# Optimization experiments

Measured on AMD Instinct MI355X. Metric: run time of the kernel, lower is better.

Reference implementation:

```python
import jax, jax.numpy as jnp
import numpy as np

IN_F, HID, N_CLS = 128, 256, 2
N_NODES, N_EDGES = 50000, 800000


def setup_inputs() -> dict:
    key = jax.random.key(0)
    ks = jax.random.split(key, 8)
    x = jax.random.normal(ks[0], (N_NODES, IN_F), dtype=jnp.float32)
    edge_index = jax.random.randint(ks[1], (2, N_EDGES), 0, N_NODES, dtype=jnp.int64)
    # Linear params (torch nn.Linear: y = x @ W.T + b), uniform(-1/sqrt(fan_in), ..)
    def lin(k, out_f, in_f):
        k1, k2 = jax.random.split(k)
        bound = 1.0 / np.sqrt(in_f)
        W = jax.random.uniform(k1, (out_f, in_f), minval=-bound, maxval=bound, dtype=jnp.float32)
        b = jax.random.uniform(k2, (out_f,), minval=-bound, maxval=bound, dtype=jnp.float32)
        return W, b
    W1, b1 = lin(ks[2], HID, IN_F)
    W2, b2 = lin(ks[3], HID // 2, HID)
    W3, b3 = lin(ks[4], N_CLS, HID // 2)
    return {"x": x, "edge_index": edge_index, "n_nodes": N_NODES,
            "W1": W1, "b1": b1, "W2": W2, "b2": b2, "W3": W3, "b3": b3}


def _gcn_layer(x, row, col, deg_inv, n_nodes, W, b):
    # gather neighbor features, scatter-add into destinations, degree-normalize
    agg = jax.ops.segment_sum(x[row], col, num_segments=n_nodes)  # [N, F]
    agg = agg * deg_inv[:, None]
    return agg @ W.T + b


def reference(x, edge_index, n_nodes, W1, b1, W2, b2, W3, b3):
    row, col = edge_index[0], edge_index[1]
    deg = jax.ops.segment_sum(jnp.ones_like(col, dtype=x.dtype), col, num_segments=n_nodes)
    deg_inv = 1.0 / jnp.maximum(deg, 1.0)  # bincount().clamp(min=1)
    h = jax.nn.relu(_gcn_layer(x, row, col, deg_inv, n_nodes, W1, b1))
    # dropout is identity in eval mode
    h = jax.nn.relu(_gcn_layer(h, row, col, deg_inv, n_nodes, W2, b2))
    return h @ W3.T + b3  # [N, num_classes]
```

## Files before the change

### kernel.cpp

```cpp
#include <hip/hip_runtime.h>
#include <hip/hip_fp16.h>

#define IN_F 128
#define HID 256
#define HID2 128
#define MAXDEG 64
#define NPART 8

typedef __attribute__((ext_vector_type(8))) _Float16 f16x8;
typedef __attribute__((ext_vector_type(4))) float f32x4;

__global__ __launch_bounds__(256) void prep(
        const float* __restrict__ x,
        const float* __restrict__ W1, const float* __restrict__ W2,
        ushort* __restrict__ xh, ushort* __restrict__ w1h, ushort* __restrict__ w1l,
        ushort* __restrict__ w2h, ushort* __restrict__ w2l,
        int* __restrict__ fill, int N) {
    int gid = blockIdx.x * 256 + threadIdx.x, gsz = gridDim.x * 256;
    for (int i = gid; i < N; i += gsz) fill[i] = 0;
    int t8 = N * IN_F / 8;
    for (int i = gid; i < t8; i += gsz) {
        const float4* s4 = (const float4*)x + (size_t)i * 2;
        float4 f0 = s4[0], f1 = s4[1];
        uint4 o;
        o.x = __half_as_ushort(__float2half(f0.x)) | ((unsigned)__half_as_ushort(__float2half(f0.y)) << 16);
        o.y = __half_as_ushort(__float2half(f0.z)) | ((unsigned)__half_as_ushort(__float2half(f0.w)) << 16);
        o.z = __half_as_ushort(__float2half(f1.x)) | ((unsigned)__half_as_ushort(__float2half(f1.y)) << 16);
        o.w = __half_as_ushort(__float2half(f1.z)) | ((unsigned)__half_as_ushort(__float2half(f1.w)) << 16);
        ((uint4*)xh)[i] = o;
    }
    int nw = HID * IN_F + HID2 * HID;
    for (int i = gid; i < nw; i += gsz) {
        bool first = i < HID * IN_F;
        int j = first ? i : i - HID * IN_F;
        float f = first ? W1[j] : W2[j];
        __half h = __float2half(f);
        __half lo = __float2half(f - __half2float(h));
        if (first) { w1h[j] = __half_as_ushort(h); w1l[j] = __half_as_ushort(lo); }
        else       { w2h[j] = __half_as_ushort(h); w2l[j] = __half_as_ushort(lo); }
    }
}

__global__ __launch_bounds__(256) void fill_csr(const int* __restrict__ row,
                                                const int* __restrict__ col,
                                                int* __restrict__ fill,
                                                ushort* __restrict__ csr,
                                                int E, int npp) {
    int part = blockIdx.x & (NPART - 1);
    int bi   = blockIdx.x >> 3;
    int bpp  = gridDim.x >> 3;
    int lo = part * npp, hi = lo + npp;
    for (int e = bi * 256 + threadIdx.x; e < E; e += bpp * 256) {
        int c = col[e];
        if (c >= lo && c < hi) {
            int p = atomicAdd(&fill[c], 1);
            if (p < MAXDEG) csr[(size_t)c * MAXDEG + p] = (ushort)row[e];
        }
    }
}

__device__ __forceinline__ void add4h(float4& a, uint2 v) {
    float2 f0 = __half22float2(*(const __half2*)&v.x);
    float2 f1 = __half22float2(*(const __half2*)&v.y);
    a.x += f0.x; a.y += f0.y; a.z += f1.x; a.w += f1.y;
}

__global__ __launch_bounds__(256) void agg_gather(const ushort* __restrict__ xh,
                                                  const int* __restrict__ deg,
                                                  const ushort* __restrict__ csr,
                                                  ushort* __restrict__ outh, int N) {
    int w = threadIdx.x >> 6, lane = threadIdx.x & 63;
    int n = blockIdx.x * 4 + w;
    if (n >= N) return;
    int d = deg[n]; if (d > MAXDEG) d = MAXDEG;
    int s = n * MAXDEG, e = s + d;
    int half = lane >> 5, l = lane & 31;
    const uint2* xv = (const uint2*)xh;
    float4 a0 = {0,0,0,0}, a1 = {0,0,0,0}, a2 = {0,0,0,0}, a3 = {0,0,0,0};
    int i = s;
    for (; i + 7 < e; i += 8) {
        int s0 = csr[i + half], s1 = csr[i + 2 + half];
        int s2 = csr[i + 4 + half], s3 = csr[i + 6 + half];
        uint2 v0 = xv[(size_t)s0 * 32 + l];
        uint2 v1 = xv[(size_t)s1 * 32 + l];
        uint2 v2 = xv[(size_t)s2 * 32 + l];
        uint2 v3 = xv[(size_t)s3 * 32 + l];
        add4h(a0, v0); add4h(a1, v1); add4h(a2, v2); add4h(a3, v3);
    }
    for (; i + 1 < e; i += 2) {
        add4h(a0, xv[(size_t)csr[i + half] * 32 + l]);
    }
    if (i < e && half == 0) {
        add4h(a0, xv[(size_t)csr[i] * 32 + l]);
    }
    a0.x += a1.x + a2.x + a3.x; a0.y += a1.y + a2.y + a3.y;
    a0.z += a1.z + a2.z + a3.z; a0.w += a1.w + a2.w + a3.w;
    a0.x += __shfl_xor(a0.x, 32, 64);
    a0.y += __shfl_xor(a0.y, 32, 64);
    a0.z += __shfl_xor(a0.z, 32, 64);
    a0.w += __shfl_xor(a0.w, 32, 64);
    if (half == 0) {
        float dinv = 1.f / fmaxf((float)d, 1.f);
        uint2 o;
        o.x = __half_as_ushort(__float2half(a0.x * dinv)) |
              ((unsigned)__half_as_ushort(__float2half(a0.y * dinv)) << 16);
        o.y = __half_as_ushort(__float2half(a0.z * dinv)) |
              ((unsigned)__half_as_ushort(__float2half(a0.w * dinv)) << 16);
        ((uint2*)outh)[(size_t)n * 32 + l] = o;
    }
}

__global__ __launch_bounds__(256, 2) void gemm_fused(const ushort* __restrict__ A,
                                                  const ushort* __restrict__ W1h,
                                                  const ushort* __restrict__ W1l,
                                                  const ushort* __restrict__ W2h,
                                                  const ushort* __restrict__ W2l,
                                                  const float* __restrict__ b1,
                                                  ushort* __restrict__ Z,
                                                  int M) {
    __shared__ _Float16 hs[64][HID + 8];
    int t = threadIdx.x;
    int wv = t >> 6, l = t & 63;
    int r = l & 15, q = l >> 4;
    int m0 = blockIdx.x * 64;
    const _Float16* Af = (const _Float16*)A;

    {
        int n0 = wv * 64;
        f16x8 WAh[4][4], WAl[4][4];
#pragma unroll
        for (int k4 = 0; k4 < 4; k4++) {
            int kf = k4 * 32 + q * 8;
#pragma unroll
            for (int j = 0; j < 4; j++) {
                size_t wo = (size_t)(n0 + 16 * j + r) * IN_F + kf;
                WAh[k4][j] = *(const f16x8*)((const _Float16*)W1h + wo);
                WAl[k4][j] = *(const f16x8*)((const _Float16*)W1l + wo);
            }
        }
        asm volatile("" ::: "memory");
        f32x4 acc[4][4];
#pragma unroll
        for (int i = 0; i < 4; i++)
#pragma unroll
            for (int j = 0; j < 4; j++) acc[i][j] = (f32x4){0.f, 0.f, 0.f, 0.f};
#pragma unroll
        for (int k4 = 0; k4 < 4; k4++) {
            int kf = k4 * 32 + q * 8;
            f16x8 a[4];
#pragma unroll
            for (int i = 0; i < 4; i++) {
                int m = m0 + 16 * i + r;
                if (m > M - 1) m = M - 1;
                a[i] = *(const f16x8*)(Af + (size_t)m * IN_F + kf);
            }
#pragma unroll
            for (int i = 0; i < 4; i++)
#pragma unroll
                for (int j = 0; j < 4; j++) {
                    acc[i][j] = __builtin_amdgcn_mfma_f32_16x16x32_f16(a[i], WAh[k4][j], acc[i][j], 0, 0, 0);
                    acc[i][j] = __builtin_amdgcn_mfma_f32_16x16x32_f16(a[i], WAl[k4][j], acc[i][j], 0, 0, 0);
                }
        }
#pragma unroll
        for (int j = 0; j < 4; j++) {
            int n = n0 + 16 * j + r;
            float bo = b1[n];
#pragma unroll
            for (int i = 0; i < 4; i++)
#pragma unroll
                for (int reg = 0; reg < 4; reg++) {
                    int mr = 16 * i + q * 4 + reg;
                    hs[mr][n] = (_Float16)fmaxf(acc[i][j][reg] + bo, 0.f);
                }
        }
    }
    __syncthreads();

    {
        int mb = (wv >> 1) * 32, n0 = (wv & 1) * 64;
        f32x4 acc[2][4];
#pragma unroll
        for (int i = 0; i < 2; i++)
#pragma unroll
            for (int j = 0; j < 4; j++) acc[i][j] = (f32x4){0.f, 0.f, 0.f, 0.f};
#pragma unroll
        for (int khalf = 0; khalf < 2; khalf++) {
            f16x8 WBh[4][4], WBl[4][4];
#pragma unroll
            for (int k4 = 0; k4 < 4; k4++) {
                int kf = khalf * 128 + k4 * 32 + q * 8;
#pragma unroll
                for (int j = 0; j < 4; j++) {
                    size_t wo = (size_t)(n0 + 16 * j + r) * HID + kf;
                    WBh[k4][j] = *(const f16x8*)((const _Float16*)W2h + wo);
                    WBl[k4][j] = *(const f16x8*)((const _Float16*)W2l + wo);
                }
            }
            asm volatile("" ::: "memory");
#pragma unroll
            for (int k4 = 0; k4 < 4; k4++) {
                int kf = khalf * 128 + k4 * 32 + q * 8;
                f16x8 a[2];
#pragma unroll
                for (int i = 0; i < 2; i++)
                    a[i] = *(const f16x8*)&hs[mb + 16 * i + r][kf];
#pragma unroll
                for (int i = 0; i < 2; i++)
#pragma unroll
                    for (int j = 0; j < 4; j++) {
                        acc[i][j] = __builtin_amdgcn_mfma_f32_16x16x32_f16(a[i], WBh[k4][j], acc[i][j], 0, 0, 0);
                        acc[i][j] = __builtin_amdgcn_mfma_f32_16x16x32_f16(a[i], WBl[k4][j], acc[i][j], 0, 0, 0);
                    }
            }
        }
#pragma unroll
        for (int i = 0; i < 2; i++)
#pragma unroll
            for (int reg = 0; reg < 4; reg++) {
                int m = m0 + mb + 16 * i + q * 4 + reg;
                if (m < M) {
#pragma unroll
                    for (int j = 0; j < 4; j++) {
                        int n = n0 + 16 * j + r;
                        Z[(size_t)m * HID2 + n] = __half_as_ushort(__float2half(acc[i][j][reg]));
                    }
                }
            }
    }
}

__global__ __launch_bounds__(256) void agg2_out(const ushort* __restrict__ zh,
                                                const int* __restrict__ deg,
                                                const ushort* __restrict__ csr,
                                                const float* __restrict__ b2,
                                                const float* __restrict__ W3,
                                                const float* __restrict__ b3,
                                                float* __restrict__ out, int N) {
    int w = threadIdx.x >> 6, lane = threadIdx.x & 63;
    int n = blockIdx.x * 4 + w;
    if (n >= N) return;
    int d = deg[n]; if (d > MAXDEG) d = MAXDEG;
    int s = n * MAXDEG, e = s + d;
    int half = lane >> 5, l = lane & 31;
    const uint2* zv = (const uint2*)zh;
    float4 a0 = {0,0,0,0}, a1 = {0,0,0,0}, a2 = {0,0,0,0}, a3 = {0,0,0,0};
    int i = s;
    for (; i + 7 < e; i += 8) {
        int s0 = csr[i + half], s1 = csr[i + 2 + half];
        int s2 = csr[i + 4 + half], s3 = csr[i + 6 + half];
        uint2 v0 = zv[(size_t)s0 * 32 + l];
        uint2 v1 = zv[(size_t)s1 * 32 + l];
        uint2 v2 = zv[(size_t)s2 * 32 + l];
        uint2 v3 = zv[(size_t)s3 * 32 + l];
        add4h(a0, v0); add4h(a1, v1); add4h(a2, v2); add4h(a3, v3);
    }
    for (; i + 1 < e; i += 2) {
        add4h(a0, zv[(size_t)csr[i + half] * 32 + l]);
    }
    if (i < e && half == 0) {
        add4h(a0, zv[(size_t)csr[i] * 32 + l]);
    }
    a0.x += a1.x + a2.x + a3.x; a0.y += a1.y + a2.y + a3.y;
    a0.z += a1.z + a2.z + a3.z; a0.w += a1.w + a2.w + a3.w;
    a0.x += __shfl_xor(a0.x, 32, 64);
    a0.y += __shfl_xor(a0.y, 32, 64);
    a0.z += __shfl_xor(a0.z, 32, 64);
    a0.w += __shfl_xor(a0.w, 32, 64);
    float dinv = 1.f / fmaxf((float)d, 1.f);
    float4 bb = ((const float4*)b2)[l];
    float4 ww = ((const float4*)W3)[half * 32 + l];
    float hx = fmaxf(a0.x * dinv + bb.x, 0.f);
    float hy = fmaxf(a0.y * dinv + bb.y, 0.f);
    float hz = fmaxf(a0.z * dinv + bb.z, 0.f);
    float hw = fmaxf(a0.w * dinv + bb.w, 0.f);
    float p = hx * ww.x + hy * ww.y + hz * ww.z + hw * ww.w;
#pragma unroll
    for (int d2 = 16; d2 > 0; d2 >>= 1) p += __shfl_xor(p, d2, 64);
    if (l == 0) out[(size_t)n * 2 + half] = p + b3[half];
}

extern "C" void kernel_launch(void* const* d_in, const int* in_sizes, int n_in,
                              void* d_out, int out_size, void* d_ws, size_t ws_size,
                              hipStream_t stream) {
    const float* x  = (const float*)d_in[0];
    const int*   ei = (const int*)d_in[1];
    const float* W1 = (const float*)d_in[3];
    const float* b1 = (const float*)d_in[4];
    const float* W2 = (const float*)d_in[5];
    const float* b2 = (const float*)d_in[6];
    const float* W3 = (const float*)d_in[7];
    const float* b3 = (const float*)d_in[8];
    float* out = (float*)d_out;

    int N = in_sizes[0] / IN_F;
    int E = in_sizes[1] / 2;
    const int* row = ei;
    const int* col = ei + E;

    char* base = (char*)d_ws;
    size_t off = 0;
    auto alloc = [&](size_t bytes) -> void* {
        off = (off + 255) & ~(size_t)255;
        void* p = base + off;
        off += bytes;
        return p;
    };
    int*    fill = (int*)alloc((size_t)N * 4);
    ushort* csr  = (ushort*)alloc((size_t)N * MAXDEG * 2);
    ushort* xh   = (ushort*)alloc((size_t)N * IN_F * 2);
    ushort* f2h  = (ushort*)alloc((size_t)N * IN_F * 2);
    ushort* z2h  = (ushort*)alloc((size_t)N * HID2 * 2);
    ushort* w1h  = (ushort*)alloc(HID * IN_F * 2);
    ushort* w1l  = (ushort*)alloc(HID * IN_F * 2);
    ushort* w2h  = (ushort*)alloc(HID2 * HID * 2);
    ushort* w2l  = (ushort*)alloc(HID2 * HID * 2);

    int npp = (N + NPART - 1) / NPART;
    prep<<<2048, 256, 0, stream>>>(x, W1, W2, xh, w1h, w1l, w2h, w2l, fill, N);
    fill_csr<<<2048, 256, 0, stream>>>(row, col, fill, csr, E, npp);
    agg_gather<<<(N + 3) / 4, 256, 0, stream>>>(xh, fill, csr, f2h, N);
    gemm_fused<<<(N + 63) / 64, 256, 0, stream>>>(f2h, w1h, w1l, w2h, w2l, b1, z2h, N);
    agg2_out<<<(N + 3) / 4, 256, 0, stream>>>(z2h, fill, csr, b2, W3, b3, out, N);
}
```

Before: 247.6 us.

## Split fused two-layer GEMM into separate LDS-staged kernels with swizzled tiles

Replaces the single fused GEMM, which kept the layer-1 output in LDS, with two kernels. Each kernel stages its activation tile in XOR-swizzled shared memory and streams the hi/lo weight slices through LDS with register prefetch. The goal is to cut register pressure and the per-wave global weight loads of the fused version. In exchange it writes and rereads a 50000x256 fp16 intermediate through global memory, adds a kernel launch, and adds two barriers per k-chunk.

```diff
diff --git a/kernel.cpp b/kernel.cpp
--- a/kernel.cpp
+++ b/kernel.cpp
@@ -110,124 +110,193 @@
     }
 }
 
-__global__ __launch_bounds__(256, 2) void gemm_fused(const ushort* __restrict__ A,
-                                                  const ushort* __restrict__ W1h,
-                                                  const ushort* __restrict__ W1l,
-                                                  const ushort* __restrict__ W2h,
-                                                  const ushort* __restrict__ W2l,
-                                                  const float* __restrict__ b1,
-                                                  ushort* __restrict__ Z,
-                                                  int M) {
-    __shared__ _Float16 hs[64][HID + 8];
+__global__ __launch_bounds__(256) void gemm1(const ushort* __restrict__ A,
+                                             const ushort* __restrict__ W1h,
+                                             const ushort* __restrict__ W1l,
+                                             const float* __restrict__ b1,
+                                             ushort* __restrict__ H, int M) {
+    __shared__ uint4 AsBuf[64 * 16];
+    __shared__ uint4 WsBuf[2 * 256 * 4];
+    ushort* As = (ushort*)AsBuf;
+    ushort* Ws = (ushort*)WsBuf;
     int t = threadIdx.x;
-    int wv = t >> 6, l = t & 63;
-    int r = l & 15, q = l >> 4;
-    int m0 = blockIdx.x * 64;
-    const _Float16* Af = (const _Float16*)A;
+    int wv = t >> 6, l = t & 63, r = l & 15, q = l >> 4;
+    int m0 = blockIdx.x * 64, n0 = wv * 64;
+    int sw = (r & 7) << 4;
 
     {
-        int n0 = wv * 64;
-        f16x8 WAh[4][4], WAl[4][4];
-#pragma unroll
-        for (int k4 = 0; k4 < 4; k4++) {
-            int kf = k4 * 32 + q * 8;
-#pragma unroll
-            for (int j = 0; j < 4; j++) {
-                size_t wo = (size_t)(n0 + 16 * j + r) * IN_F + kf;
-                WAh[k4][j] = *(const f16x8*)((const _Float16*)W1h + wo);
-                WAl[k4][j] = *(const f16x8*)((const _Float16*)W1l + wo);
-            }
-        }
-        asm volatile("" ::: "memory");
-        f32x4 acc[4][4];
-#pragma unroll
-        for (int i = 0; i < 4; i++)
-#pragma unroll
-            for (int j = 0; j < 4; j++) acc[i][j] = (f32x4){0.f, 0.f, 0.f, 0.f};
-#pragma unroll
-        for (int k4 = 0; k4 < 4; k4++) {
-            int kf = k4 * 32 + q * 8;
-            f16x8 a[4];
-#pragma unroll
-            for (int i = 0; i < 4; i++) {
-                int m = m0 + 16 * i + r;
-                if (m > M - 1) m = M - 1;
-                a[i] = *(const f16x8*)(Af + (size_t)m * IN_F + kf);
-            }
-#pragma unroll
-            for (int i = 0; i < 4; i++)
-#pragma unroll
-                for (int j = 0; j < 4; j++) {
-                    acc[i][j] = __builtin_amdgcn_mfma_f32_16x16x32_f16(a[i], WAh[k4][j], acc[i][j], 0, 0, 0);
-                    acc[i][j] = __builtin_amdgcn_mfma_f32_16x16x32_f16(a[i], WAl[k4][j], acc[i][j], 0, 0, 0);
-                }
-        }
+        int row = t & 63, seg = t >> 6;
+        int m = m0 + row; if (m > M - 1) m = M - 1;
+        const uint4* g = (const uint4*)(A + (size_t)m * IN_F) + seg * 4;
+        uint4 v0 = g[0], v1 = g[1], v2 = g[2], v3 = g[3];
+        char* db = (char*)As + row * 256;
+        int rs = (row & 7) << 4;
+        *(uint4*)(db + ((seg * 64 +  0) ^ rs)) = v0;
+        *(uint4*)(db + ((seg * 64 + 16) ^ rs)) = v1;
+        *(uint4*)(db + ((seg * 64 + 32) ^ rs)) = v2;
+        *(uint4*)(db + ((seg * 64 + 48) ^ rs)) = v3;
+    }
+    {
+        const uint4* gh = (const uint4*)(W1h + (size_t)t * IN_F);
+        const uint4* gl = (const uint4*)(W1l + (size_t)t * IN_F);
+        uint4* dh = (uint4*)Ws + t * 4;
+        uint4* dl = (uint4*)Ws + (256 + t) * 4;
+#pragma unroll
+        for (int s = 0; s < 4; s++) { dh[s] = gh[s]; dl[s] = gl[s]; }
+    }
+    __syncthreads();
+
+    f32x4 acc[4][4];
+#pragma unroll
+    for (int i = 0; i < 4; i++)
+#pragma unroll
+        for (int j = 0; j < 4; j++) acc[i][j] = (f32x4){0.f, 0.f, 0.f, 0.f};
+
+    for (int kc = 0; kc < 4; kc++) {
+        uint4 ph[4], pl[4];
+        if (kc < 3) {
+            const uint4* gh = (const uint4*)(W1h + (size_t)t * IN_F + (kc + 1) * 32);
+            const uint4* gl = (const uint4*)(W1l + (size_t)t * IN_F + (kc + 1) * 32);
+#pragma unroll
+            for (int s = 0; s < 4; s++) { ph[s] = gh[s]; pl[s] = gl[s]; }
+        }
+        f16x8 wh[4], wl[4], a[4];
 #pragma unroll
         for (int j = 0; j < 4; j++) {
             int n = n0 + 16 * j + r;
-            float bo = b1[n];
-#pragma unroll
-            for (int i = 0; i < 4; i++)
-#pragma unroll
-                for (int reg = 0; reg < 4; reg++) {
-                    int mr = 16 * i + q * 4 + reg;
-                    hs[mr][n] = (_Float16)fmaxf(acc[i][j][reg] + bo, 0.f);
-                }
-        }
+            wh[j] = *(const f16x8*)(Ws + (size_t)n * 32 + q * 8);
+            wl[j] = *(const f16x8*)(Ws + 8192 + (size_t)n * 32 + q * 8);
+        }
+#pragma unroll
+        for (int i = 0; i < 4; i++) {
+            int row = 16 * i + r;
+            a[i] = *(const f16x8*)((const char*)As + row * 256 + ((kc * 64 + q * 16) ^ sw));
+        }
+#pragma unroll
+        for (int i = 0; i < 4; i++)
+#pragma unroll
+            for (int j = 0; j < 4; j++) {
+                acc[i][j] = __builtin_amdgcn_mfma_f32_16x16x32_f16(a[i], wh[j], acc[i][j], 0, 0, 0);
+                acc[i][j] = __builtin_amdgcn_mfma_f32_16x16x32_f16(a[i], wl[j], acc[i][j], 0, 0, 0);
+            }
+        if (kc < 3) {
+            __syncthreads();
+            uint4* dh = (uint4*)Ws + t * 4;
+            uint4* dl = (uint4*)Ws + (256 + t) * 4;
+#pragma unroll
+            for (int s = 0; s < 4; s++) { dh[s] = ph[s]; dl[s] = pl[s]; }
+            __syncthreads();
+        }
+    }
+
+#pragma unroll
+    for (int j = 0; j < 4; j++) {
+        int n = n0 + 16 * j + r;
+        float bo = b1[n];
+#pragma unroll
+        for (int i = 0; i < 4; i++)
+#pragma unroll
+            for (int reg = 0; reg < 4; reg++) {
+                int m = m0 + 16 * i + q * 4 + reg;
+                if (m < M)
+                    H[(size_t)m * HID + n] =
+                        __half_as_ushort(__float2half(fmaxf(acc[i][j][reg] + bo, 0.f)));
+            }
+    }
+}
+
+__global__ __launch_bounds__(256) void gemm2(const ushort* __restrict__ Hh,
+                                             const ushort* __restrict__ W2h,
+                                             const ushort* __restrict__ W2l,
+                                             ushort* __restrict__ Z, int M) {
+    __shared__ uint4 AsBuf[64 * 32];
+    __shared__ uint4 WsBuf[2 * 128 * 4];
+    ushort* As = (ushort*)AsBuf;
+    ushort* Ws = (ushort*)WsBuf;
+    int t = threadIdx.x;
+    int wv = t >> 6, l = t & 63, r = l & 15, q = l >> 4;
+    int m0 = blockIdx.x * 64;
+    int mb = (wv >> 1) * 32, n0 = (wv & 1) * 64;
+    int sw = (r & 7) << 4;
+
+    {
+        int row = t & 63, seg = t >> 6;
+        int m = m0 + row; if (m > M - 1) m = M - 1;
+        const uint4* g = (const uint4*)(Hh + (size_t)m * HID) + seg * 8;
+        char* db = (char*)As + row * 512;
+        int rs = (row & 7) << 4;
+#pragma unroll
+        for (int s = 0; s < 8; s++) {
+            uint4 v = g[s];
+            *(uint4*)(db + ((seg * 128 + s * 16) ^ rs)) = v;
+        }
+    }
+    {
+        int plane = t >> 7, row = t & 127;
+        const ushort* src = (plane ? W2l : W2h) + (size_t)row * HID;
+        const uint4* g = (const uint4*)src;
+        uint4* d = (uint4*)Ws + (plane * 128 + row) * 4;
+#pragma unroll
+        for (int s = 0; s < 4; s++) d[s] = g[s];
     }
     __syncthreads();
 
-    {
-        int mb = (wv >> 1) * 32, n0 = (wv & 1) * 64;
-        f32x4 acc[2][4];
+    f32x4 acc[2][4];
+#pragma unroll
+    for (int i = 0; i < 2; i++)
+#pragma unroll
+        for (int j = 0; j < 4; j++) acc[i][j] = (f32x4){0.f, 0.f, 0.f, 0.f};
+
+    for (int kc = 0; kc < 8; kc++) {
+        uint4 pw[4];
+        int plane = t >> 7, wrow = t & 127;
+        if (kc < 7) {
+            const ushort* src = (plane ? W2l : W2h) + (size_t)wrow * HID + (kc + 1) * 32;
+            const uint4* g = (const uint4*)src;
+#pragma unroll
+            for (int s = 0; s < 4; s++) pw[s] = g[s];
+        }
+        f16x8 wh[4], wl[4], a[2];
+#pragma unroll
+        for (int j = 0; j < 4; j++) {
+            int n = n0 + 16 * j + r;
+            wh[j] = *(const f16x8*)(Ws + (size_t)n * 32 + q * 8);
+            wl[j] = *(const f16x8*)(Ws + 4096 + (size_t)n * 32 + q * 8);
+        }
+#pragma unroll
+        for (int i = 0; i < 2; i++) {
+            int row = mb + 16 * i + r;
+            a[i] = *(const f16x8*)((const char*)As + row * 512 + ((kc * 64 + q * 16) ^ sw));
+        }
 #pragma unroll
         for (int i = 0; i < 2; i++)
 #pragma unroll
-            for (int j = 0; j < 4; j++) acc[i][j] = (f32x4){0.f, 0.f, 0.f, 0.f};
-#pragma unroll
-        for (int khalf = 0; khalf < 2; khalf++) {
-            f16x8 WBh[4][4], WBl[4][4];
-#pragma unroll
-            for (int k4 = 0; k4 < 4; k4++) {
-                int kf = khalf * 128 + k4 * 32 + q * 8;
+            for (int j = 0; j < 4; j++) {
+                acc[i][j] = __builtin_amdgcn_mfma_f32_16x16x32_f16(a[i], wh[j], acc[i][j], 0, 0, 0);
+                acc[i][j] = __builtin_amdgcn_mfma_f32_16x16x32_f16(a[i], wl[j], acc[i][j], 0, 0, 0);
+            }
+        if (kc < 7) {
+            __syncthreads();
+            uint4* d = (uint4*)Ws + (plane * 128 + wrow) * 4;
+#pragma unroll
+            for (int s = 0; s < 4; s++) d[s] = pw[s];
+            __syncthreads();
+        }
+    }
+
+#pragma unroll
+    for (int i = 0; i < 2; i++)
+#pragma unroll
+        for (int reg = 0; reg < 4; reg++) {
+            int m = m0 + mb + 16 * i + q * 4 + reg;
+            if (m < M) {
 #pragma unroll
                 for (int j = 0; j < 4; j++) {
-                    size_t wo = (size_t)(n0 + 16 * j + r) * HID + kf;
-                    WBh[k4][j] = *(const f16x8*)((const _Float16*)W2h + wo);
-                    WBl[k4][j] = *(const f16x8*)((const _Float16*)W2l + wo);
+                    int n = n0 + 16 * j + r;
+                    Z[(size_t)m * HID2 + n] = __half_as_ushort(__float2half(acc[i][j][reg]));
                 }
             }
-            asm volatile("" ::: "memory");
-#pragma unroll
-            for (int k4 = 0; k4 < 4; k4++) {
-                int kf = khalf * 128 + k4 * 32 + q * 8;
-                f16x8 a[2];
-#pragma unroll
-                for (int i = 0; i < 2; i++)
-                    a[i] = *(const f16x8*)&hs[mb + 16 * i + r][kf];
-#pragma unroll
-                for (int i = 0; i < 2; i++)
-#pragma unroll
-                    for (int j = 0; j < 4; j++) {
-                        acc[i][j] = __builtin_amdgcn_mfma_f32_16x16x32_f16(a[i], WBh[k4][j], acc[i][j], 0, 0, 0);
-                        acc[i][j] = __builtin_amdgcn_mfma_f32_16x16x32_f16(a[i], WBl[k4][j], acc[i][j], 0, 0, 0);
-                    }
-            }
-        }
-#pragma unroll
-        for (int i = 0; i < 2; i++)
-#pragma unroll
-            for (int reg = 0; reg < 4; reg++) {
-                int m = m0 + mb + 16 * i + q * 4 + reg;
-                if (m < M) {
-#pragma unroll
-                    for (int j = 0; j < 4; j++) {
-                        int n = n0 + 16 * j + r;
-                        Z[(size_t)m * HID2 + n] = __half_as_ushort(__float2half(acc[i][j][reg]));
-                    }
-                }
-            }
-    }
+        }
 }
 
 __global__ __launch_bounds__(256) void agg2_out(const ushort* __restrict__ zh,
@@ -310,6 +379,7 @@
     ushort* csr  = (ushort*)alloc((size_t)N * MAXDEG * 2);
     ushort* xh   = (ushort*)alloc((size_t)N * IN_F * 2);
     ushort* f2h  = (ushort*)alloc((size_t)N * IN_F * 2);
+    ushort* h1   = (ushort*)alloc((size_t)N * HID * 2);
     ushort* z2h  = (ushort*)alloc((size_t)N * HID2 * 2);
     ushort* w1h  = (ushort*)alloc(HID * IN_F * 2);
     ushort* w1l  = (ushort*)alloc(HID * IN_F * 2);
@@ -317,9 +387,11 @@
     ushort* w2l  = (ushort*)alloc(HID2 * HID * 2);
 
     int npp = (N + NPART - 1) / NPART;
+    int gb = (N + 63) / 64;
     prep<<<2048, 256, 0, stream>>>(x, W1, W2, xh, w1h, w1l, w2h, w2l, fill, N);
     fill_csr<<<2048, 256, 0, stream>>>(row, col, fill, csr, E, npp);
     agg_gather<<<(N + 3) / 4, 256, 0, stream>>>(xh, fill, csr, f2h, N);
-    gemm_fused<<<(N + 63) / 64, 256, 0, stream>>>(f2h, w1h, w1l, w2h, w2l, b1, z2h, N);
+    gemm1<<<gb, 256, 0, stream>>>(f2h, w1h, w1l, b1, h1, N);
+    gemm2<<<gb, 256, 0, stream>>>(h1, w2h, w2l, z2h, N);
     agg2_out<<<(N + 3) / 4, 256, 0, stream>>>(z2h, fill, csr, b2, W3, b3, out, N);
 }
```

New measurement: 303.3 us. +22.5%, slower.

## Split fused GEMM across 8 waves with register double-buffered K-step loads

Applied to the files above, without the earlier changes.

The fused two-layer GEMM block grows from 4 to 8 waves, so each wave owns a narrower 32-column slice of the output. The whole-K weight fragment arrays held in registers are replaced by a per-K-step double buffer that prefetches the next activation and weight fragments while the current MFMAs run. This cuts register pressure to allow more resident waves and overlaps global load latency with compute. In exchange, weight fragments are reloaded more often per block, and the activation tile is now read by more waves.

```diff
diff --git a/kernel.cpp b/kernel.cpp
--- a/kernel.cpp
+++ b/kernel.cpp
@@ -110,7 +110,7 @@
     }
 }
 
-__global__ __launch_bounds__(256, 2) void gemm_fused(const ushort* __restrict__ A,
+__global__ __launch_bounds__(512, 2) void gemm_fused(const ushort* __restrict__ A,
                                                   const ushort* __restrict__ W1h,
                                                   const ushort* __restrict__ W1l,
                                                   const ushort* __restrict__ W2h,
@@ -126,44 +126,59 @@
     const _Float16* Af = (const _Float16*)A;
 
     {
-        int n0 = wv * 64;
-        f16x8 WAh[4][4], WAl[4][4];
+        int n0 = wv * 32;
+        int nA = n0 + r, nB = n0 + 16 + r;
+        const _Float16* whp = (const _Float16*)W1h;
+        const _Float16* wlp = (const _Float16*)W1l;
+        int mrow[4];
+#pragma unroll
+        for (int i = 0; i < 4; i++) {
+            int m = m0 + 16 * i + r;
+            if (m > M - 1) m = M - 1;
+            mrow[i] = m;
+        }
+        f32x4 acc[4][2];
+#pragma unroll
+        for (int i = 0; i < 4; i++)
+#pragma unroll
+            for (int j = 0; j < 2; j++) acc[i][j] = (f32x4){0.f, 0.f, 0.f, 0.f};
+
+        f16x8 a[4], wh[2], wl[2];
+#pragma unroll
+        for (int i = 0; i < 4; i++) a[i] = *(const f16x8*)(Af + (size_t)mrow[i] * IN_F + q * 8);
+        wh[0] = *(const f16x8*)(whp + (size_t)nA * IN_F + q * 8);
+        wh[1] = *(const f16x8*)(whp + (size_t)nB * IN_F + q * 8);
+        wl[0] = *(const f16x8*)(wlp + (size_t)nA * IN_F + q * 8);
+        wl[1] = *(const f16x8*)(wlp + (size_t)nB * IN_F + q * 8);
+
 #pragma unroll
         for (int k4 = 0; k4 < 4; k4++) {
-            int kf = k4 * 32 + q * 8;
-#pragma unroll
-            for (int j = 0; j < 4; j++) {
-                size_t wo = (size_t)(n0 + 16 * j + r) * IN_F + kf;
-                WAh[k4][j] = *(const f16x8*)((const _Float16*)W1h + wo);
-                WAl[k4][j] = *(const f16x8*)((const _Float16*)W1l + wo);
-            }
-        }
-        asm volatile("" ::: "memory");
-        f32x4 acc[4][4];
-#pragma unroll
-        for (int i = 0; i < 4; i++)
-#pragma unroll
-            for (int j = 0; j < 4; j++) acc[i][j] = (f32x4){0.f, 0.f, 0.f, 0.f};
-#pragma unroll
-        for (int k4 = 0; k4 < 4; k4++) {
-            int kf = k4 * 32 + q * 8;
-            f16x8 a[4];
-#pragma unroll
-            for (int i = 0; i < 4; i++) {
-                int m = m0 + 16 * i + r;
-                if (m > M - 1) m = M - 1;
-                a[i] = *(const f16x8*)(Af + (size_t)m * IN_F + kf);
+            f16x8 na[4], nwh[2], nwl[2];
+            if (k4 < 3) {
+                int kf = (k4 + 1) * 32 + q * 8;
+#pragma unroll
+                for (int i = 0; i < 4; i++) na[i] = *(const f16x8*)(Af + (size_t)mrow[i] * IN_F + kf);
+                nwh[0] = *(const f16x8*)(whp + (size_t)nA * IN_F + kf);
+                nwh[1] = *(const f16x8*)(whp + (size_t)nB * IN_F + kf);
+                nwl[0] = *(const f16x8*)(wlp + (size_t)nA * IN_F + kf);
+                nwl[1] = *(const f16x8*)(wlp + (size_t)nB * IN_F + kf);
             }
 #pragma unroll
             for (int i = 0; i < 4; i++)
 #pragma unroll
-                for (int j = 0; j < 4; j++) {
-                    acc[i][j] = __builtin_amdgcn_mfma_f32_16x16x32_f16(a[i], WAh[k4][j], acc[i][j], 0, 0, 0);
-                    acc[i][j] = __builtin_amdgcn_mfma_f32_16x16x32_f16(a[i], WAl[k4][j], acc[i][j], 0, 0, 0);
+                for (int j = 0; j < 2; j++) {
+                    acc[i][j] = __builtin_amdgcn_mfma_f32_16x16x32_f16(a[i], wh[j], acc[i][j], 0, 0, 0);
+                    acc[i][j] = __builtin_amdgcn_mfma_f32_16x16x32_f16(a[i], wl[j], acc[i][j], 0, 0, 0);
                 }
-        }
-#pragma unroll
-        for (int j = 0; j < 4; j++) {
+            if (k4 < 3) {
+#pragma unroll
+                for (int i = 0; i < 4; i++) a[i] = na[i];
+                wh[0] = nwh[0]; wh[1] = nwh[1];
+                wl[0] = nwl[0]; wl[1] = nwl[1];
+            }
+        }
+#pragma unroll
+        for (int j = 0; j < 2; j++) {
             int n = n0 + 16 * j + r;
             float bo = b1[n];
 #pragma unroll
@@ -178,40 +193,47 @@
     __syncthreads();
 
     {
-        int mb = (wv >> 1) * 32, n0 = (wv & 1) * 64;
-        f32x4 acc[2][4];
+        int mb = (wv >> 2) * 32, n0 = (wv & 3) * 32;
+        int nA = n0 + r, nB = n0 + 16 + r;
+        const _Float16* whp = (const _Float16*)W2h;
+        const _Float16* wlp = (const _Float16*)W2l;
+        f32x4 acc[2][2];
 #pragma unroll
         for (int i = 0; i < 2; i++)
 #pragma unroll
-            for (int j = 0; j < 4; j++) acc[i][j] = (f32x4){0.f, 0.f, 0.f, 0.f};
-#pragma unroll
-        for (int khalf = 0; khalf < 2; khalf++) {
-            f16x8 WBh[4][4], WBl[4][4];
-#pragma unroll
-            for (int k4 = 0; k4 < 4; k4++) {
-                int kf = khalf * 128 + k4 * 32 + q * 8;
-#pragma unroll
-                for (int j = 0; j < 4; j++) {
-                    size_t wo = (size_t)(n0 + 16 * j + r) * HID + kf;
-                    WBh[k4][j] = *(const f16x8*)((const _Float16*)W2h + wo);
-                    WBl[k4][j] = *(const f16x8*)((const _Float16*)W2l + wo);
+            for (int j = 0; j < 2; j++) acc[i][j] = (f32x4){0.f, 0.f, 0.f, 0.f};
+
+        f16x8 wh[2], wl[2];
+        wh[0] = *(const f16x8*)(whp + (size_t)nA * HID + q * 8);
+        wh[1] = *(const f16x8*)(whp + (size_t)nB * HID + q * 8);
+        wl[0] = *(const f16x8*)(wlp + (size_t)nA * HID + q * 8);
+        wl[1] = *(const f16x8*)(wlp + (size_t)nB * HID + q * 8);
+
+#pragma unroll
+        for (int kk = 0; kk < 8; kk++) {
+            f16x8 nwh[2], nwl[2];
+            if (kk < 7) {
+                int kf = (kk + 1) * 32 + q * 8;
+                nwh[0] = *(const f16x8*)(whp + (size_t)nA * HID + kf);
+                nwh[1] = *(const f16x8*)(whp + (size_t)nB * HID + kf);
+                nwl[0] = *(const f16x8*)(wlp + (size_t)nA * HID + kf);
+                nwl[1] = *(const f16x8*)(wlp + (size_t)nB * HID + kf);
+            }
+            int kf = kk * 32 + q * 8;
+            f16x8 a[2];
+#pragma unroll
+            for (int i = 0; i < 2; i++)
+                a[i] = *(const f16x8*)&hs[mb + 16 * i + r][kf];
+#pragma unroll
+            for (int i = 0; i < 2; i++)
+#pragma unroll
+                for (int j = 0; j < 2; j++) {
+                    acc[i][j] = __builtin_amdgcn_mfma_f32_16x16x32_f16(a[i], wh[j], acc[i][j], 0, 0, 0);
+                    acc[i][j] = __builtin_amdgcn_mfma_f32_16x16x32_f16(a[i], wl[j], acc[i][j], 0, 0, 0);
                 }
-            }
-            asm volatile("" ::: "memory");
-#pragma unroll
-            for (int k4 = 0; k4 < 4; k4++) {
-                int kf = khalf * 128 + k4 * 32 + q * 8;
-                f16x8 a[2];
-#pragma unroll
-                for (int i = 0; i < 2; i++)
-                    a[i] = *(const f16x8*)&hs[mb + 16 * i + r][kf];
-#pragma unroll
-                for (int i = 0; i < 2; i++)
-#pragma unroll
-                    for (int j = 0; j < 4; j++) {
-                        acc[i][j] = __builtin_amdgcn_mfma_f32_16x16x32_f16(a[i], WBh[k4][j], acc[i][j], 0, 0, 0);
-                        acc[i][j] = __builtin_amdgcn_mfma_f32_16x16x32_f16(a[i], WBl[k4][j], acc[i][j], 0, 0, 0);
-                    }
+            if (kk < 7) {
+                wh[0] = nwh[0]; wh[1] = nwh[1];
+                wl[0] = nwl[0]; wl[1] = nwl[1];
             }
         }
 #pragma unroll
@@ -221,7 +243,7 @@
                 int m = m0 + mb + 16 * i + q * 4 + reg;
                 if (m < M) {
 #pragma unroll
-                    for (int j = 0; j < 4; j++) {
+                    for (int j = 0; j < 2; j++) {
                         int n = n0 + 16 * j + r;
                         Z[(size_t)m * HID2 + n] = __half_as_ushort(__float2half(acc[i][j][reg]));
                     }
@@ -320,6 +342,6 @@
     prep<<<2048, 256, 0, stream>>>(x, W1, W2, xh, w1h, w1l, w2h, w2l, fill, N);
     fill_csr<<<2048, 256, 0, stream>>>(row, col, fill, csr, E, npp);
     agg_gather<<<(N + 3) / 4, 256, 0, stream>>>(xh, fill, csr, f2h, N);
-    gemm_fused<<<(N + 63) / 64, 256, 0, stream>>>(f2h, w1h, w1l, w2h, w2l, b1, z2h, N);
+    gemm_fused<<<(N + 63) / 64, 512, 0, stream>>>(f2h, w1h, w1l, w2h, w2l, b1, z2h, N);
     agg2_out<<<(N + 3) / 4, 256, 0, stream>>>(z2h, fill, csr, b2, W3, b3, out, N);
 }
```

Measured after the change: 251.1 us. About the same (+1.4%).

## Make fused GEMM persistent with register-resident prepacked weights and swizzled LDS

Applied to the files above, without the earlier changes.

The fused two-layer GEMM becomes a persistent kernel of 256 blocks with 512 threads. Each block loads the W1 and W2 hi/lo fragments into registers once, from a fragment-major layout prepacked by the prep kernel, and then loops over 64-row tiles. A tiles are staged through XOR-swizzled shared memory, and the swizzle is also applied to the hidden-activation buffer to avoid bank conflicts. This removes the repeated per-block weight reloads from global memory. In exchange it adds heavy register pressure (launch bounds 512,1) and an extra barrier per tile.

```diff
diff --git a/kernel.cpp b/kernel.cpp
--- a/kernel.cpp
+++ b/kernel.cpp
@@ -13,8 +13,7 @@
 __global__ __launch_bounds__(256) void prep(
         const float* __restrict__ x,
         const float* __restrict__ W1, const float* __restrict__ W2,
-        ushort* __restrict__ xh, ushort* __restrict__ w1h, ushort* __restrict__ w1l,
-        ushort* __restrict__ w2h, ushort* __restrict__ w2l,
+        ushort* __restrict__ xh, ushort* __restrict__ w1p, ushort* __restrict__ w2p,
         int* __restrict__ fill, int N) {
     int gid = blockIdx.x * 256 + threadIdx.x, gsz = gridDim.x * 256;
     for (int i = gid; i < N; i += gsz) fill[i] = 0;
@@ -29,15 +28,27 @@
         o.w = __half_as_ushort(__float2half(f1.z)) | ((unsigned)__half_as_ushort(__float2half(f1.w)) << 16);
         ((uint4*)xh)[i] = o;
     }
-    int nw = HID * IN_F + HID2 * HID;
-    for (int i = gid; i < nw; i += gsz) {
-        bool first = i < HID * IN_F;
-        int j = first ? i : i - HID * IN_F;
-        float f = first ? W1[j] : W2[j];
-        __half h = __float2half(f);
-        __half lo = __float2half(f - __half2float(h));
-        if (first) { w1h[j] = __half_as_ushort(h); w1l[j] = __half_as_ushort(lo); }
-        else       { w2h[j] = __half_as_ushort(h); w2l[j] = __half_as_ushort(lo); }
+    for (int i = gid; i < 65536; i += gsz) {
+        int l = (i >> 3) & 63, plane = (i >> 9) & 1, j = (i >> 10) & 1;
+        int k4 = (i >> 11) & 3, wvv = (i >> 13) & 7;
+        int q = l >> 4, rr = l & 15;
+        int n = wvv * 32 + 16 * j + rr;
+        int k = k4 * 32 + q * 8 + (i & 7);
+        float f = W1[n * IN_F + k];
+        __half hh = __float2half(f);
+        w1p[i] = plane ? __half_as_ushort(__float2half(f - __half2float(hh)))
+                       : __half_as_ushort(hh);
+    }
+    for (int i = gid; i < 65536; i += gsz) {
+        int l = (i >> 3) & 63, plane = (i >> 9) & 1, j = (i >> 10) & 1;
+        int kk = (i >> 11) & 7, g = (i >> 14) & 3;
+        int q = l >> 4, rr = l & 15;
+        int n = g * 32 + 16 * j + rr;
+        int k = kk * 32 + q * 8 + (i & 7);
+        float f = W2[n * HID + k];
+        __half hh = __float2half(f);
+        w2p[i] = plane ? __half_as_ushort(__float2half(f - __half2float(hh)))
+                       : __half_as_ushort(hh);
     }
 }
 
@@ -110,120 +121,122 @@
     }
 }
 
-__global__ __launch_bounds__(256, 2) void gemm_fused(const ushort* __restrict__ A,
-                                                  const ushort* __restrict__ W1h,
-                                                  const ushort* __restrict__ W1l,
-                                                  const ushort* __restrict__ W2h,
-                                                  const ushort* __restrict__ W2l,
-                                                  const float* __restrict__ b1,
-                                                  ushort* __restrict__ Z,
-                                                  int M) {
-    __shared__ _Float16 hs[64][HID + 8];
+__global__ __launch_bounds__(512, 1) void gemm_fused(const ushort* __restrict__ A,
+                                                     const ushort* __restrict__ w1p,
+                                                     const ushort* __restrict__ w2p,
+                                                     const float* __restrict__ b1,
+                                                     ushort* __restrict__ Z,
+                                                     int M, int nt) {
+    __shared__ uint4 AbufV[1024];
+    __shared__ uint4 hsbV[2048];
+    char* Abuf = (char*)AbufV;
+    char* hsb  = (char*)hsbV;
     int t = threadIdx.x;
-    int wv = t >> 6, l = t & 63;
-    int r = l & 15, q = l >> 4;
-    int m0 = blockIdx.x * 64;
-    const _Float16* Af = (const _Float16*)A;
-
-    {
-        int n0 = wv * 64;
-        f16x8 WAh[4][4], WAl[4][4];
+    int wv = t >> 6, l = t & 63, r = l & 15, q = l >> 4;
+
+    f16x8 w1f[4][2][2];
+#pragma unroll
+    for (int k4 = 0; k4 < 4; k4++)
+#pragma unroll
+        for (int j = 0; j < 2; j++)
+#pragma unroll
+            for (int p = 0; p < 2; p++)
+                w1f[k4][j][p] = *(const f16x8*)((const _Float16*)w1p +
+                                  ((((wv * 4 + k4) * 2 + j) * 2 + p) * 512 + l * 8));
+    int g = wv & 3;
+    f16x8 w2f[8][2][2];
+#pragma unroll
+    for (int kk = 0; kk < 8; kk++)
+#pragma unroll
+        for (int j = 0; j < 2; j++)
+#pragma unroll
+            for (int p = 0; p < 2; p++)
+                w2f[kk][j][p] = *(const f16x8*)((const _Float16*)w2p +
+                                  ((((g * 8 + kk) * 2 + j) * 2 + p) * 512 + l * 8));
+
+    int nA0 = wv * 32;
+    float bo0 = b1[nA0 + r], bo1 = b1[nA0 + 16 + r];
+    int mbB = (wv >> 2) * 32, nB0 = (wv & 3) * 32;
+
+    for (int tile = blockIdx.x; tile < nt; tile += gridDim.x) {
+        int m0 = tile * 64;
+#pragma unroll
+        for (int s = 0; s < 2; s++) {
+            int u = s * 8192 + t * 16;
+            int arow = u >> 8, seg = (u >> 4) & 15;
+            int m = m0 + arow; if (m > M - 1) m = M - 1;
+            uint4 v = *(const uint4*)((const char*)A + (size_t)m * 256 + seg * 16);
+            *(uint4*)(Abuf + arow * 256 + ((seg ^ (arow & 7)) << 4)) = v;
+        }
+        __syncthreads();
+
+        f32x4 acc[4][2];
+#pragma unroll
+        for (int i = 0; i < 4; i++)
+#pragma unroll
+            for (int j = 0; j < 2; j++) acc[i][j] = (f32x4){0.f, 0.f, 0.f, 0.f};
 #pragma unroll
         for (int k4 = 0; k4 < 4; k4++) {
-            int kf = k4 * 32 + q * 8;
-#pragma unroll
-            for (int j = 0; j < 4; j++) {
-                size_t wo = (size_t)(n0 + 16 * j + r) * IN_F + kf;
-                WAh[k4][j] = *(const f16x8*)((const _Float16*)W1h + wo);
-                WAl[k4][j] = *(const f16x8*)((const _Float16*)W1l + wo);
+            f16x8 a[4];
+#pragma unroll
+            for (int i = 0; i < 4; i++) {
+                int arow = 16 * i + r;
+                a[i] = *(const f16x8*)(Abuf + arow * 256 + (((k4 * 4 + q) ^ (arow & 7)) << 4));
             }
-        }
-        asm volatile("" ::: "memory");
-        f32x4 acc[4][4];
-#pragma unroll
-        for (int i = 0; i < 4; i++)
-#pragma unroll
-            for (int j = 0; j < 4; j++) acc[i][j] = (f32x4){0.f, 0.f, 0.f, 0.f};
-#pragma unroll
-        for (int k4 = 0; k4 < 4; k4++) {
-            int kf = k4 * 32 + q * 8;
-            f16x8 a[4];
-#pragma unroll
-            for (int i = 0; i < 4; i++) {
-                int m = m0 + 16 * i + r;
-                if (m > M - 1) m = M - 1;
-                a[i] = *(const f16x8*)(Af + (size_t)m * IN_F + kf);
-            }
 #pragma unroll
             for (int i = 0; i < 4; i++)
 #pragma unroll
-                for (int j = 0; j < 4; j++) {
-                    acc[i][j] = __builtin_amdgcn_mfma_f32_16x16x32_f16(a[i], WAh[k4][j], acc[i][j], 0, 0, 0);
-                    acc[i][j] = __builtin_amdgcn_mfma_f32_16x16x32_f16(a[i], WAl[k4][j], acc[i][j], 0, 0, 0);
+                for (int j = 0; j < 2; j++) {
+                    acc[i][j] = __builtin_amdgcn_mfma_f32_16x16x32_f16(a[i], w1f[k4][j][0], acc[i][j], 0, 0, 0);
+                    acc[i][j] = __builtin_amdgcn_mfma_f32_16x16x32_f16(a[i], w1f[k4][j][1], acc[i][j], 0, 0, 0);
                 }
         }
 #pragma unroll
-        for (int j = 0; j < 4; j++) {
-            int n = n0 + 16 * j + r;
-            float bo = b1[n];
+        for (int j = 0; j < 2; j++) {
+            float bo = j ? bo1 : bo0;
+            int n = nA0 + 16 * j + r;
 #pragma unroll
             for (int i = 0; i < 4; i++)
 #pragma unroll
                 for (int reg = 0; reg < 4; reg++) {
                     int mr = 16 * i + q * 4 + reg;
-                    hs[mr][n] = (_Float16)fmaxf(acc[i][j][reg] + bo, 0.f);
+                    *(_Float16*)(hsb + mr * 512 + ((((n >> 3) ^ (mr & 7)) << 4)) + (n & 7) * 2)
+                        = (_Float16)fmaxf(acc[i][j][reg] + bo, 0.f);
                 }
         }
-    }
-    __syncthreads();
-
-    {
-        int mb = (wv >> 1) * 32, n0 = (wv & 1) * 64;
-        f32x4 acc[2][4];
+        __syncthreads();
+
+        f32x4 accB[2][2];
 #pragma unroll
         for (int i = 0; i < 2; i++)
 #pragma unroll
-            for (int j = 0; j < 4; j++) acc[i][j] = (f32x4){0.f, 0.f, 0.f, 0.f};
-#pragma unroll
-        for (int khalf = 0; khalf < 2; khalf++) {
-            f16x8 WBh[4][4], WBl[4][4];
-#pragma unroll
-            for (int k4 = 0; k4 < 4; k4++) {
-                int kf = khalf * 128 + k4 * 32 + q * 8;
-#pragma unroll
-                for (int j = 0; j < 4; j++) {
-                    size_t wo = (size_t)(n0 + 16 * j + r) * HID + kf;
-                    WBh[k4][j] = *(const f16x8*)((const _Float16*)W2h + wo);
-                    WBl[k4][j] = *(const f16x8*)((const _Float16*)W2l + wo);
+            for (int j = 0; j < 2; j++) accB[i][j] = (f32x4){0.f, 0.f, 0.f, 0.f};
+#pragma unroll
+        for (int kk = 0; kk < 8; kk++) {
+            f16x8 a[2];
+#pragma unroll
+            for (int i = 0; i < 2; i++) {
+                int hrow = mbB + 16 * i + r;
+                a[i] = *(const f16x8*)(hsb + hrow * 512 + (((kk * 4 + q) ^ (hrow & 7)) << 4));
+            }
+#pragma unroll
+            for (int i = 0; i < 2; i++)
+#pragma unroll
+                for (int j = 0; j < 2; j++) {
+                    accB[i][j] = __builtin_amdgcn_mfma_f32_16x16x32_f16(a[i], w2f[kk][j][0], accB[i][j], 0, 0, 0);
+                    accB[i][j] = __builtin_amdgcn_mfma_f32_16x16x32_f16(a[i], w2f[kk][j][1], accB[i][j], 0, 0, 0);
                 }
-            }
-            asm volatile("" ::: "memory");
-#pragma unroll
-            for (int k4 = 0; k4 < 4; k4++) {
-                int kf = khalf * 128 + k4 * 32 + q * 8;
-                f16x8 a[2];
-#pragma unroll
-                for (int i = 0; i < 2; i++)
-                    a[i] = *(const f16x8*)&hs[mb + 16 * i + r][kf];
-#pragma unroll
-                for (int i = 0; i < 2; i++)
-#pragma unroll
-                    for (int j = 0; j < 4; j++) {
-                        acc[i][j] = __builtin_amdgcn_mfma_f32_16x16x32_f16(a[i], WBh[k4][j], acc[i][j], 0, 0, 0);
-                        acc[i][j] = __builtin_amdgcn_mfma_f32_16x16x32_f16(a[i], WBl[k4][j], acc[i][j], 0, 0, 0);
-                    }
-            }
         }
 #pragma unroll
         for (int i = 0; i < 2; i++)
 #pragma unroll
             for (int reg = 0; reg < 4; reg++) {
-                int m = m0 + mb + 16 * i + q * 4 + reg;
+                int m = m0 + mbB + 16 * i + q * 4 + reg;
                 if (m < M) {
 #pragma unroll
-                    for (int j = 0; j < 4; j++) {
-                        int n = n0 + 16 * j + r;
-                        Z[(size_t)m * HID2 + n] = __half_as_ushort(__float2half(acc[i][j][reg]));
+                    for (int j = 0; j < 2; j++) {
+                        int n = nB0 + 16 * j + r;
+                        Z[(size_t)m * HID2 + n] = __half_as_ushort(__float2half(accB[i][j][reg]));
                     }
                 }
             }
@@ -311,15 +324,14 @@
     ushort* xh   = (ushort*)alloc((size_t)N * IN_F * 2);
     ushort* f2h  = (ushort*)alloc((size_t)N * IN_F * 2);
     ushort* z2h  = (ushort*)alloc((size_t)N * HID2 * 2);
-    ushort* w1h  = (ushort*)alloc(HID * IN_F * 2);
-    ushort* w1l  = (ushort*)alloc(HID * IN_F * 2);
-    ushort* w2h  = (ushort*)alloc(HID2 * HID * 2);
-    ushort* w2l  = (ushort*)alloc(HID2 * HID * 2);
+    ushort* w1p  = (ushort*)alloc(65536 * 2);
+    ushort* w2p  = (ushort*)alloc(65536 * 2);
 
     int npp = (N + NPART - 1) / NPART;
-    prep<<<2048, 256, 0, stream>>>(x, W1, W2, xh, w1h, w1l, w2h, w2l, fill, N);
+    int nt = (N + 63) / 64;
+    prep<<<2048, 256, 0, stream>>>(x, W1, W2, xh, w1p, w2p, fill, N);
     fill_csr<<<2048, 256, 0, stream>>>(row, col, fill, csr, E, npp);
     agg_gather<<<(N + 3) / 4, 256, 0, stream>>>(xh, fill, csr, f2h, N);
-    gemm_fused<<<(N + 63) / 64, 256, 0, stream>>>(f2h, w1h, w1l, w2h, w2l, b1, z2h, N);
+    gemm_fused<<<256, 512, 0, stream>>>(f2h, w1p, w2p, b1, z2h, N, nt);
     agg2_out<<<(N + 3) / 4, 256, 0, stream>>>(z2h, fill, csr, b2, W3, b3, out, N);
 }
```

Measured after the change: 227.9 us. 1.09x faster.
